# Optimization experiments

Measured on AMD Instinct MI355X. Metric: run time of the kernel, lower is better.

## Reference

```python
import jax, jax.numpy as jnp
import numpy as np

B, T, K, H, KS = 4, 2048, 128, 8, 5
DIL = 2
PAD = (KS - 1) * DIL  # left causal pad = 8


def _conv1d(x, w, dil):
    # x: [b, c_in, t], w: [c_out, c_in, ks] -> [b, c_out, t_out]
    return jax.lax.conv_general_dilated(
        x, w, window_strides=(1,), padding='VALID',
        rhs_dilation=(dil,), dimension_numbers=('NCH', 'OIH', 'NCH'))


def setup_inputs() -> dict:
    key = jax.random.key(0)
    ks = jax.random.split(key, 8)
    s = 0.05
    return {
        'x': jax.random.normal(ks[0], (B, T, K), dtype=jnp.float32),
        'Wq': jax.random.normal(ks[1], (K * H, K, KS), dtype=jnp.float32) * s,
        'bq': jax.random.normal(ks[2], (K * H,), dtype=jnp.float32) * s,
        'Wk': jax.random.normal(ks[3], (K * H, K, KS), dtype=jnp.float32) * s,
        'bk': jax.random.normal(ks[4], (K * H,), dtype=jnp.float32) * s,
        'Wv': jax.random.normal(ks[5], (K * H, K, 1), dtype=jnp.float32) * s,
        'Wu': jax.random.normal(ks[6], (K, K * H), dtype=jnp.float32) * s,
        'bu': jax.random.normal(ks[7], (K,), dtype=jnp.float32) * s,
    }


def reference(x, Wq, bq, Wk, bk, Wv, Wu, bu):
    b, t, k = x.shape
    h = Wq.shape[0] // k
    silu = jax.nn.silu

    xt = jnp.transpose(x, (0, 2, 1))               # [b, k, t]
    xp = jnp.pad(xt, ((0, 0), (0, 0), (PAD, 0)))   # causal left pad

    # dilated convs -> view(b, k, h, t) (channel split: k outer, h inner, as in torch)
    q = silu(_conv1d(xp, Wq, DIL) + bq[None, :, None]).reshape(b, k, h, t)
    kk = silu(_conv1d(xp, Wk, DIL) + bk[None, :, None]).reshape(b, k, h, t)
    v = silu(_conv1d(xt, Wv, 1)).reshape(b, k, h, t)

    # -> (b, h, t, k)
    q = jnp.transpose(q, (0, 2, 3, 1))
    kk = jnp.transpose(kk, (0, 2, 3, 1))
    v = jnp.transpose(v, (0, 2, 3, 1))

    scale = k ** 0.25
    q = q / scale
    kk = kk / scale

    # faithful to torch: transpose(1,2) -> (b,t,h,k) then contiguous view (b*h, t, k)
    q2 = jnp.transpose(q, (0, 2, 1, 3)).reshape(b * h, t, k)
    k2 = jnp.transpose(kk, (0, 2, 1, 3)).reshape(b * h, t, k)
    v2 = jnp.transpose(v, (0, 2, 1, 3)).reshape(b * h, t, k)

    weights = jnp.einsum('mtd,msd->mts', q2, k2)   # [b*h, t, t]
    causal = jnp.triu(jnp.ones((t, t), dtype=bool), 1)  # mask_next, not diag
    weights = jnp.where(causal[None], -jnp.inf, weights)
    attn = jax.nn.softmax(weights, axis=2)
    out = jnp.einsum('mts,msd->mtd', attn, v2)     # [b*h, t, k]

    out = out.reshape(b, h, t, k).transpose(0, 2, 1, 3).reshape(b, t, k * h)
    return silu(out @ Wu.T + bu)
```

## Files before the change

kernel.cpp:

```cpp
#include <hip/hip_runtime.h>
#include <hip/hip_bf16.h>
#include <stdint.h>


typedef __attribute__((ext_vector_type(8))) short bf16x8;
typedef __attribute__((ext_vector_type(4))) float f32x4;
typedef __attribute__((ext_vector_type(4))) int   i32x4;
typedef unsigned short ushort_t;

__device__ __forceinline__ unsigned short f2bf(float x){
  union{float f; unsigned u;} v; v.f = x;
  unsigned r = v.u + 0x7FFFu + ((v.u >> 16) & 1u);
  return (unsigned short)(r >> 16);
}
__device__ __forceinline__ float silu_f(float x){ return x / (1.f + __expf(-x)); }

__device__ __forceinline__ int cvt_pk_bf16(float lo, float hi){
  int r;
  asm("v_cvt_pk_bf16_f32 %0, %1, %2" : "=v"(r) : "v"(lo), "v"(hi));
  return r;
}

__device__ __forceinline__ void async_cp16(void* lds, const void* g){
  __builtin_amdgcn_global_load_lds(
      (const __attribute__((address_space(1))) unsigned int*)g,
      (__attribute__((address_space(3))) unsigned int*)lds, 16, 0, 0);
}

__global__ __launch_bounds__(256) void prep(const float* __restrict__ Wq,
                                            const float* __restrict__ Wk,
                                            const float* __restrict__ Wv,
                                            const float* __restrict__ Wu,
                                            const float* __restrict__ x,
                                            ushort_t* __restrict__ W2p,
                                            ushort_t* __restrict__ Wvp,
                                            ushort_t* __restrict__ Wub,
                                            ushort_t* __restrict__ Xpad){
  __shared__ float row[640];
  int n = blockIdx.x;
  int tid = threadIdx.x;
  if (n < 2048){
    int qk = n >> 10, h = (n >> 7) & 7, d = n & 127;
    const float* src = (qk ? Wk : Wq) + (size_t)(d*8 + h)*640;
    if (tid < 160) *(float4*)&row[tid*4] = *(const float4*)&src[tid*4];
    __syncthreads();
    for (int rp = tid; rp < 640; rp += 256){
      int j = rp >> 7, ci = rp & 127;
      W2p[(size_t)n*640 + rp] = f2bf(row[ci*5 + j]);
    }
  } else if (n < 3072){
    int co = n - 2048;
    if (tid < 32){
      float4 v = *(const float4*)&Wv[(size_t)co*128 + tid*4];
      uint2 pv;
      pv.x = (unsigned)cvt_pk_bf16(v.x, v.y);
      pv.y = (unsigned)cvt_pk_bf16(v.z, v.w);
      *(uint2*)&Wvp[(size_t)co*128 + tid*4] = pv;
    }
  } else if (n < 3200){
    int j = n - 3072;
    float4 v = *(const float4*)&Wu[(size_t)j*1024 + tid*4];
    uint2 pv;
    pv.x = (unsigned)cvt_pk_bf16(v.x, v.y);
    pv.y = (unsigned)cvt_pk_bf16(v.z, v.w);
    *(uint2*)&Wub[(size_t)j*1024 + tid*4] = pv;
  } else {
    int idx = n - 3200;
    int b = idx / 257, rblk = idx - b*257;
    int rt = rblk*8 + (tid >> 5);
    int ci4 = (tid & 31) * 4;
    int t = rt - 8;
    uint2 val; val.x = 0u; val.y = 0u;
    if (t >= 0){
      float4 v = *(const float4*)&x[((size_t)(b*2048 + t))*128 + ci4];
      val.x = (unsigned)cvt_pk_bf16(v.x, v.y);
      val.y = (unsigned)cvt_pk_bf16(v.z, v.w);
    }
    *(uint2*)&Xpad[((size_t)(b*2056 + rt))*128 + ci4] = val;
  }
}

__global__ __launch_bounds__(256) void gemm_qkv(
    const ushort_t* __restrict__ Xpad,
    const ushort_t* __restrict__ W2p,
    const ushort_t* __restrict__ Wvp,
    const float* __restrict__ bq, const float* __restrict__ bk,
    ushort_t* __restrict__ Q2, ushort_t* __restrict__ K2,
    ushort_t* __restrict__ V2t)
{
  __shared__ ushort_t As[2][128*32] __attribute__((aligned(16)));
  __shared__ ushort_t Bs[2][128*32] __attribute__((aligned(16)));
  int bt0 = blockIdx.y * 128;
  int tid = threadIdx.x;
  int w = tid >> 6, ln = tid & 63;
  int lc = ln & 15, lg = ln >> 4;
  int mi = (w & 1) * 64, nj = (w >> 1) * 64;
  int srow = ln >> 2;
  int kseg = (ln & 3) * 8;
  int b = bt0 >> 11, tl0 = bt0 & 2047;

  f32x4 acc[4][4];
  #pragma unroll
  for (int si = 0; si < 4; si++)
    #pragma unroll
    for (int sj = 0; sj < 4; sj++) acc[si][sj] = (f32x4){0.f,0.f,0.f,0.f};

  if (blockIdx.x < 16){
    int n0 = blockIdx.x * 128;
    const ushort_t* gA = Xpad + (size_t)(b*2056 + tl0 + w*32 + srow)*128 + kseg;
    const ushort_t* gB = W2p + (size_t)(n0  + w*32 + srow)*640 + kseg;

    auto stageAB = [&](int kk, int bsel){
      int j = kk >> 2, ci0 = (kk & 3) * 32;
      int r0 = kk * 32;
      const ushort_t* a0 = gA + (size_t)(2*j)*128 + ci0;
      async_cp16(&As[bsel][w*1024],       a0);
      async_cp16(&As[bsel][w*1024 + 512], a0 + 16*128);
      async_cp16(&Bs[bsel][w*1024],       gB + r0);
      async_cp16(&Bs[bsel][w*1024 + 512], gB + r0 + 16*640);
    };

    stageAB(0, 0);
    for (int kk = 0; kk < 20; kk++){
      int bsel = kk & 1;
      if (kk + 1 < 20){
        stageAB(kk + 1, bsel ^ 1);
        asm volatile("s_waitcnt vmcnt(4)\n\ts_barrier" ::: "memory");
      } else {
        asm volatile("s_waitcnt vmcnt(0)\n\ts_barrier" ::: "memory");
      }
      bf16x8 af[4], bfr[4];
      #pragma unroll
      for (int si = 0; si < 4; si++)
        af[si] = *(const bf16x8*)&As[bsel][(mi + 16*si + lc)*32 + 8*lg];
      #pragma unroll
      for (int sj = 0; sj < 4; sj++)
        bfr[sj] = *(const bf16x8*)&Bs[bsel][(nj + 16*sj + lc)*32 + 8*lg];
      #pragma unroll
      for (int si = 0; si < 4; si++)
        #pragma unroll
        for (int sj = 0; sj < 4; sj++)
          acc[si][sj] = __builtin_amdgcn_mfma_f32_16x16x32_bf16(af[si], bfr[sj],
                                                                acc[si][sj], 0,0,0);
      asm volatile("s_barrier" ::: "memory");
    }

    const float inv_scale = 0.29730177875068026f;
    int qk = n0 >> 10, h = (n0 >> 7) & 7;
    const float* bias = qk ? bk : bq;
    ushort_t* dst = qk ? K2 : Q2;
    float bv[4];
    #pragma unroll
    for (int sj = 0; sj < 4; sj++) bv[sj] = bias[(nj + 16*sj + lc)*8 + h];

    #pragma unroll
    for (int si = 0; si < 4; si++){
      int btb = bt0 + mi + 16*si + 4*lg;
      #pragma unroll
      for (int r = 0; r < 4; r++){
        int t = btb + r;
        int bb = t >> 11, tl = t & 2047;
        size_t rowoff = ((size_t)(bb*8 + (tl >> 8))*2048 + (tl & 255)*8 + h)*128;
        #pragma unroll
        for (int sj = 0; sj < 4; sj++){
          int d = nj + 16*sj + lc;
          dst[rowoff + d] = f2bf(silu_f(acc[si][sj][r] + bv[sj]) * inv_scale);
        }
      }
    }
  } else {
    int n0 = (blockIdx.x - 16) * 128;
    const ushort_t* gA = Xpad + (size_t)(b*2056 + 8 + tl0 + w*32 + srow)*128 + kseg;
    const ushort_t* gB = Wvp  + (size_t)(n0 + w*32 + srow)*128 + kseg;

    auto stageV = [&](int kk, int bsel){
      int r0 = kk * 32;
      async_cp16(&As[bsel][w*1024],       gA + r0);
      async_cp16(&As[bsel][w*1024 + 512], gA + r0 + 16*128);
      async_cp16(&Bs[bsel][w*1024],       gB + r0);
      async_cp16(&Bs[bsel][w*1024 + 512], gB + r0 + 16*128);
    };

    stageV(0, 0);
    for (int kk = 0; kk < 4; kk++){
      int bsel = kk & 1;
      if (kk + 1 < 4){
        stageV(kk + 1, bsel ^ 1);
        asm volatile("s_waitcnt vmcnt(4)\n\ts_barrier" ::: "memory");
      } else {
        asm volatile("s_waitcnt vmcnt(0)\n\ts_barrier" ::: "memory");
      }
      bf16x8 af[4], bfr[4];
      #pragma unroll
      for (int si = 0; si < 4; si++)
        af[si] = *(const bf16x8*)&As[bsel][(mi + 16*si + lc)*32 + 8*lg];
      #pragma unroll
      for (int sj = 0; sj < 4; sj++)
        bfr[sj] = *(const bf16x8*)&Bs[bsel][(nj + 16*sj + lc)*32 + 8*lg];
      #pragma unroll
      for (int si = 0; si < 4; si++)
        #pragma unroll
        for (int sj = 0; sj < 4; sj++)
          acc[si][sj] = __builtin_amdgcn_mfma_f32_16x16x32_bf16(af[si], bfr[sj],
                                                                acc[si][sj], 0,0,0);
      asm volatile("s_barrier" ::: "memory");
    }

    #pragma unroll
    for (int si = 0; si < 4; si++){
      int btb = bt0 + mi + 16*si + 4*lg;
      #pragma unroll
      for (int r = 0; r < 4; r++){
        int t = btb + r;
        int bb = t >> 11, tl = t & 2047;
        int mm = bb*8 + (tl >> 8);
        int tpb = (tl & 255)*8;
        #pragma unroll
        for (int sj = 0; sj < 4; sj++){
          int co = n0 + nj + 16*sj + lc;
          int d = co >> 3, hh = co & 7;
          V2t[((size_t)mm*128 + d)*2048 + tpb + hh] = f2bf(silu_f(acc[si][sj][r]));
        }
      }
    }
  }
}

__global__ __launch_bounds__(256) void attn(
    const ushort_t* __restrict__ Q2,
    const ushort_t* __restrict__ K2,
    const ushort_t* __restrict__ V2t,
    ushort_t* __restrict__ O2)
{
  __shared__ i32x4 kbuf[2][1024];
  __shared__ i32x4 vbuf[2][1024];

  int bid = blockIdx.x;
  int m   = ((bid & 7) << 2) | ((bid >> 3) & 3);
  int ip  = bid >> 5;
  int tid = threadIdx.x;
  int w = tid >> 6, l = tid & 63;
  int lc = l & 15, lg = l >> 4;

  int iA = 31 - ip, iB = ip;
  int ntA = iA + 1;
  const int nt = 33;

  const size_t mQ = (size_t)m * 2048;
  const ushort_t* Kbase = K2  + mQ * 128;
  const ushort_t* Vbase = V2t + (size_t)m * 128 * 2048;
  int hb = m & 7, bI = m >> 3;

  int psel[4];
  #pragma unroll
  for (int w2 = 0; w2 < 4; w2++)
    psel[w2] = ((((2*(lg & 1) + (w2 >> 1)) << 4) | lc) << 2);

  auto stage = [&](int s0, int bsel){
    const ushort_t* krow = Kbase + (size_t)(s0 + w*16 + lc)*128 + 8*lg;
    #pragma unroll
    for (int c = 0; c < 4; c++)
      async_cp16(&kbuf[bsel][(w*4 + c)*64], krow + 32*c);
    #pragma unroll
    for (int j = 0; j < 4; j++){
      int dt = w*2 + (j >> 1);
      const ushort_t* vrow = Vbase + (size_t)(dt*16 + lc)*2048
                             + s0 + (j & 1)*32 + 8*lg;
      async_cp16(&vbuf[bsel][(w*4 + j)*64], vrow);
    }
  };

  int qb = iA*64 + w*16;
  bf16x8 qfrag[4];
  {
    const ushort_t* qp = Q2 + (mQ + qb + lc)*128 + 8*lg;
    #pragma unroll
    for (int c = 0; c < 4; c++) qfrag[c] = *(const bf16x8*)(qp + 32*c);
  }
  f32x4 oacc[8];
  #pragma unroll
  for (int dt = 0; dt < 8; dt++) oacc[dt] = (f32x4){0.f,0.f,0.f,0.f};
  float lrow = 0.f;

  const float LOG2E = 1.4426950408889634f;
  const float EOFF  = -11.541560327111707f;

  stage(0, 0);

  for (int step = 0; step < nt; step++){
    if (step == ntA){
      float lt = lrow;
      lt += __shfl_xor(lt, 16);
      lt += __shfl_xor(lt, 32);
      float invl = 1.f / lt;
      size_t obase = ((size_t)(bI*2048 + qb + lc))*1024 + hb*128 + 4*lg;
      #pragma unroll
      for (int dt = 0; dt < 8; dt++){
        uint2 val;
        val.x = (unsigned)cvt_pk_bf16(oacc[dt][0]*invl, oacc[dt][1]*invl);
        val.y = (unsigned)cvt_pk_bf16(oacc[dt][2]*invl, oacc[dt][3]*invl);
        *(uint2*)&O2[obase + 16*dt] = val;
      }
      qb = iB*64 + w*16;
      const ushort_t* qp = Q2 + (mQ + qb + lc)*128 + 8*lg;
      #pragma unroll
      for (int c = 0; c < 4; c++) qfrag[c] = *(const bf16x8*)(qp + 32*c);
      #pragma unroll
      for (int dt = 0; dt < 8; dt++) oacc[dt] = (f32x4){0.f,0.f,0.f,0.f};
      lrow = 0.f;
    }
    int local = (step < ntA) ? step : step - ntA;
    bool isLast = (step == ntA - 1) || (step == nt - 1);
    int s0 = local * 64;
    int bsel = step & 1;

    if (step + 1 < nt){
      int nl = (step + 1 < ntA) ? step + 1 : step + 1 - ntA;
      stage(nl*64, bsel ^ 1);
      asm volatile("s_waitcnt vmcnt(8)\n\ts_barrier" ::: "memory");
    } else {
      asm volatile("s_waitcnt vmcnt(0)\n\ts_barrier" ::: "memory");
    }

    f32x4 sacc[4];
    #pragma unroll
    for (int st = 0; st < 4; st++){
      f32x4 a2 = (f32x4){0.f,0.f,0.f,0.f};
      #pragma unroll
      for (int c = 0; c < 4; c++){
        bf16x8 kf = *(bf16x8*)&kbuf[bsel][(st*4 + c)*64 + l];
        a2 = __builtin_amdgcn_mfma_f32_16x16x32_bf16(kf, qfrag[c], a2, 0, 0, 0);
      }
      sacc[st] = a2;
    }
    if (isLast){
      int qg = qb + lc;
      #pragma unroll
      for (int st = 0; st < 4; st++)
        #pragma unroll
        for (int r = 0; r < 4; r++){
          int sg = s0 + st*16 + 4*lg + r;
          if (sg > qg) sacc[st][r] = -1e30f;
        }
    }

    float p_[4][4];
    #pragma unroll
    for (int st = 0; st < 4; st++)
      #pragma unroll
      for (int r = 0; r < 4; r++){
        float sv = fminf(fmaf(sacc[st][r], LOG2E, EOFF), 108.f);
        float pv = __builtin_amdgcn_exp2f(sv);
        p_[st][r] = pv;
        lrow += pv;
      }

    #pragma unroll
    for (int ks = 0; ks < 2; ks++){
      int pk0[2], pk1[2];
      #pragma unroll
      for (int pa = 0; pa < 2; pa++){
        pk0[pa] = cvt_pk_bf16(p_[2*ks][2*pa],   p_[2*ks][2*pa+1]);
        pk1[pa] = cvt_pk_bf16(p_[2*ks+1][2*pa], p_[2*ks+1][2*pa+1]);
      }
      union { int i[4]; bf16x8 v; } bfr;
      #pragma unroll
      for (int w2 = 0; w2 < 4; w2++){
        int v0 = __builtin_amdgcn_ds_bpermute(psel[w2], pk0[w2 & 1]);
        int v1 = __builtin_amdgcn_ds_bpermute(psel[w2], pk1[w2 & 1]);
        bfr.i[w2] = (lg >> 1) ? v1 : v0;
      }
      #pragma unroll
      for (int dt = 0; dt < 8; dt++){
        bf16x8 vf = *(bf16x8*)&vbuf[bsel][(dt*2 + ks)*64 + l];
        oacc[dt] = __builtin_amdgcn_mfma_f32_16x16x32_bf16(vf, bfr.v, oacc[dt], 0, 0, 0);
      }
    }
    asm volatile("s_barrier" ::: "memory");
  }

  float lt = lrow;
  lt += __shfl_xor(lt, 16);
  lt += __shfl_xor(lt, 32);
  float invl = 1.f / lt;
  size_t obase = ((size_t)(bI*2048 + qb + lc))*1024 + hb*128 + 4*lg;
  #pragma unroll
  for (int dt = 0; dt < 8; dt++){
    uint2 val;
    val.x = (unsigned)cvt_pk_bf16(oacc[dt][0]*invl, oacc[dt][1]*invl);
    val.y = (unsigned)cvt_pk_bf16(oacc[dt][2]*invl, oacc[dt][3]*invl);
    *(uint2*)&O2[obase + 16*dt] = val;
  }
}

__global__ __launch_bounds__(256) void finalmm(
    const ushort_t* __restrict__ O2,
    const ushort_t* __restrict__ Wub,
    const float* __restrict__ bu,
    float* __restrict__ out)
{
  __shared__ ushort_t As[2][32*32]  __attribute__((aligned(16)));
  __shared__ ushort_t Bs[2][128*32] __attribute__((aligned(16)));
  int bt0 = blockIdx.x * 32;
  int tid = threadIdx.x;
  int w = tid >> 6, ln = tid & 63;
  int lc = ln & 15, lg = ln >> 4;
  int nj = w * 32;
  int srow = ln >> 2;
  int kseg = (ln & 3) * 8;

  f32x4 acc[2][2];
  #pragma unroll
  for (int si = 0; si < 2; si++)
    #pragma unroll
    for (int sj = 0; sj < 2; sj++) acc[si][sj] = (f32x4){0.f,0.f,0.f,0.f};

  const ushort_t* gA = O2  + (size_t)(bt0 + (w & 1)*16 + srow)*1024 + kseg;
  const ushort_t* gB = Wub + (size_t)(w*32 + srow)*1024 + kseg;

  auto stageF = [&](int kk, int bsel){
    int r0 = kk * 32;
    if (w < 2) async_cp16(&As[bsel][w*512], gA + r0);
    async_cp16(&Bs[bsel][w*1024],       gB + r0);
    async_cp16(&Bs[bsel][w*1024 + 512], gB + r0 + 16*1024);
  };

  stageF(0, 0);
  for (int kk = 0; kk < 32; kk++){
    int bsel = kk & 1;
    if (kk + 1 < 32){
      stageF(kk + 1, bsel ^ 1);
      asm volatile("s_waitcnt vmcnt(2)\n\ts_barrier" ::: "memory");
    } else {
      asm volatile("s_waitcnt vmcnt(0)\n\ts_barrier" ::: "memory");
    }
    bf16x8 af[2], bfr[2];
    #pragma unroll
    for (int si = 0; si < 2; si++)
      af[si] = *(const bf16x8*)&As[bsel][(16*si + lc)*32 + 8*lg];
    #pragma unroll
    for (int sj = 0; sj < 2; sj++)
      bfr[sj] = *(const bf16x8*)&Bs[bsel][(nj + 16*sj + lc)*32 + 8*lg];
    #pragma unroll
    for (int si = 0; si < 2; si++)
      #pragma unroll
      for (int sj = 0; sj < 2; sj++)
        acc[si][sj] = __builtin_amdgcn_mfma_f32_16x16x32_bf16(af[si], bfr[sj],
                                                              acc[si][sj], 0,0,0);
    asm volatile("s_barrier" ::: "memory");
  }

  float bv[2];
  #pragma unroll
  for (int sj = 0; sj < 2; sj++) bv[sj] = bu[nj + 16*sj + lc];
  #pragma unroll
  for (int si = 0; si < 2; si++)
    #pragma unroll
    for (int r = 0; r < 4; r++){
      int t = bt0 + 16*si + 4*lg + r;
      #pragma unroll
      for (int sj = 0; sj < 2; sj++)
        out[(size_t)t*128 + nj + 16*sj + lc] = silu_f(acc[si][sj][r] + bv[sj]);
    }
}

extern "C" void kernel_launch(void* const* d_in, const int* in_sizes, int n_in,
                              void* d_out, int out_size, void* d_ws, size_t ws_size,
                              hipStream_t stream) {
  const float* x  = (const float*)d_in[0];
  const float* Wq = (const float*)d_in[1];
  const float* bq = (const float*)d_in[2];
  const float* Wk = (const float*)d_in[3];
  const float* bk = (const float*)d_in[4];
  const float* Wv = (const float*)d_in[5];
  const float* Wu = (const float*)d_in[6];
  const float* bu = (const float*)d_in[7];
  float* out = (float*)d_out;

  char* ws = (char*)d_ws;
  ushort_t* Q2   = (ushort_t*)(ws + 0);
  ushort_t* K2   = (ushort_t*)(ws + 16777216);
  ushort_t* V2t  = (ushort_t*)(ws + 33554432);
  ushort_t* O2   = (ushort_t*)(ws + 50331648);
  ushort_t* Xpad = (ushort_t*)(ws + 67108864);
  ushort_t* W2p  = (ushort_t*)(ws + 70254592);
  ushort_t* Wvp  = (ushort_t*)(ws + 73400320);
  ushort_t* Wub  = (ushort_t*)(ws + 74448896);

  prep<<<dim3(4228, 1, 1), 256, 0, stream>>>(Wq, Wk, Wv, Wu, x,
                                             W2p, Wvp, Wub, Xpad);

  gemm_qkv<<<dim3(24, 64, 1), 256, 0, stream>>>(Xpad, W2p, Wvp, bq, bk,
                                                Q2, K2, V2t);

  attn<<<dim3(512, 1, 1), 256, 0, stream>>>(Q2, K2, V2t, O2);
  finalmm<<<dim3(256, 1, 1), 256, 0, stream>>>(O2, Wub, bu, out);
}
```

Before: 203.0 us.

## Process both paired query tiles concurrently to share K/V tile loads

The attention kernel previously walked the K/V sequence twice per block, once for the long query tile and once for the short one, staging 33 K/V tiles in total. It now loads K/V tiles only for the longer causal range and, during the first iB+1 steps, computes scores and PV products for both query tiles against the same staged tiles. This roughly halves global-to-LDS staging and barrier count per block. In exchange it doubles the accumulator and Q-fragment registers (two oacc sets of 8 f32x4), which may raise VGPR pressure and lower occupancy.

```diff
diff --git a/kernel.cpp b/kernel.cpp
--- a/kernel.cpp
+++ b/kernel.cpp
@@ -242,9 +242,10 @@
   int w = tid >> 6, l = tid & 63;
   int lc = l & 15, lg = l >> 4;
 
-  int iA = 31 - ip, iB = ip;
-  int ntA = iA + 1;
-  const int nt = 33;
+  int iA = 31 - ip;
+  int iB = ip;
+  int nsteps = iA + 1;
+  int ndual  = iB + 1;
 
   const size_t mQ = (size_t)m * 2048;
   const ushort_t* Kbase = K2  + mQ * 128;
@@ -270,126 +271,195 @@
     }
   };
 
-  int qb = iA*64 + w*16;
-  bf16x8 qfrag[4];
+  int qbA = iA*64 + w*16;
+  int qbB = iB*64 + w*16;
+  bf16x8 qf[2][4];
   {
-    const ushort_t* qp = Q2 + (mQ + qb + lc)*128 + 8*lg;
-    #pragma unroll
-    for (int c = 0; c < 4; c++) qfrag[c] = *(const bf16x8*)(qp + 32*c);
-  }
-  f32x4 oacc[8];
+    const ushort_t* qpA = Q2 + (mQ + qbA + lc)*128 + 8*lg;
+    const ushort_t* qpB = Q2 + (mQ + qbB + lc)*128 + 8*lg;
+    #pragma unroll
+    for (int c = 0; c < 4; c++){
+      qf[0][c] = *(const bf16x8*)(qpA + 32*c);
+      qf[1][c] = *(const bf16x8*)(qpB + 32*c);
+    }
+  }
+  f32x4 oacc[2][8];
   #pragma unroll
-  for (int dt = 0; dt < 8; dt++) oacc[dt] = (f32x4){0.f,0.f,0.f,0.f};
-  float lrow = 0.f;
+  for (int dt = 0; dt < 8; dt++){
+    oacc[0][dt] = (f32x4){0.f,0.f,0.f,0.f};
+    oacc[1][dt] = (f32x4){0.f,0.f,0.f,0.f};
+  }
+  float lrow0 = 0.f, lrow1 = 0.f;
 
   const float LOG2E = 1.4426950408889634f;
   const float EOFF  = -11.541560327111707f;
 
   stage(0, 0);
 
-  for (int step = 0; step < nt; step++){
-    if (step == ntA){
-      float lt = lrow;
-      lt += __shfl_xor(lt, 16);
-      lt += __shfl_xor(lt, 32);
-      float invl = 1.f / lt;
-      size_t obase = ((size_t)(bI*2048 + qb + lc))*1024 + hb*128 + 4*lg;
-      #pragma unroll
-      for (int dt = 0; dt < 8; dt++){
-        uint2 val;
-        val.x = (unsigned)cvt_pk_bf16(oacc[dt][0]*invl, oacc[dt][1]*invl);
-        val.y = (unsigned)cvt_pk_bf16(oacc[dt][2]*invl, oacc[dt][3]*invl);
-        *(uint2*)&O2[obase + 16*dt] = val;
-      }
-      qb = iB*64 + w*16;
-      const ushort_t* qp = Q2 + (mQ + qb + lc)*128 + 8*lg;
-      #pragma unroll
-      for (int c = 0; c < 4; c++) qfrag[c] = *(const bf16x8*)(qp + 32*c);
-      #pragma unroll
-      for (int dt = 0; dt < 8; dt++) oacc[dt] = (f32x4){0.f,0.f,0.f,0.f};
-      lrow = 0.f;
-    }
-    int local = (step < ntA) ? step : step - ntA;
-    bool isLast = (step == ntA - 1) || (step == nt - 1);
-    int s0 = local * 64;
-    int bsel = step & 1;
-
-    if (step + 1 < nt){
-      int nl = (step + 1 < ntA) ? step + 1 : step + 1 - ntA;
-      stage(nl*64, bsel ^ 1);
+  for (int s = 0; s < nsteps; s++){
+    int bsel = s & 1;
+    int s0 = s * 64;
+
+    if (s + 1 < nsteps){
+      stage(s0 + 64, bsel ^ 1);
       asm volatile("s_waitcnt vmcnt(8)\n\ts_barrier" ::: "memory");
     } else {
       asm volatile("s_waitcnt vmcnt(0)\n\ts_barrier" ::: "memory");
     }
 
-    f32x4 sacc[4];
-    #pragma unroll
-    for (int st = 0; st < 4; st++){
-      f32x4 a2 = (f32x4){0.f,0.f,0.f,0.f};
-      #pragma unroll
-      for (int c = 0; c < 4; c++){
-        bf16x8 kf = *(bf16x8*)&kbuf[bsel][(st*4 + c)*64 + l];
-        a2 = __builtin_amdgcn_mfma_f32_16x16x32_bf16(kf, qfrag[c], a2, 0, 0, 0);
-      }
-      sacc[st] = a2;
-    }
-    if (isLast){
-      int qg = qb + lc;
+    if (s < ndual){
+      f32x4 sacc0[4], sacc1[4];
+      #pragma unroll
+      for (int st = 0; st < 4; st++){
+        f32x4 a0 = (f32x4){0.f,0.f,0.f,0.f};
+        f32x4 a1 = (f32x4){0.f,0.f,0.f,0.f};
+        #pragma unroll
+        for (int c = 0; c < 4; c++){
+          bf16x8 kf = *(bf16x8*)&kbuf[bsel][(st*4 + c)*64 + l];
+          a0 = __builtin_amdgcn_mfma_f32_16x16x32_bf16(kf, qf[0][c], a0, 0, 0, 0);
+          a1 = __builtin_amdgcn_mfma_f32_16x16x32_bf16(kf, qf[1][c], a1, 0, 0, 0);
+        }
+        sacc0[st] = a0; sacc1[st] = a1;
+      }
+      if (s == iB){
+        int qg = qbB + lc;
+        #pragma unroll
+        for (int st = 0; st < 4; st++)
+          #pragma unroll
+          for (int r = 0; r < 4; r++){
+            int sg = s0 + st*16 + 4*lg + r;
+            if (sg > qg) sacc1[st][r] = -1e30f;
+          }
+      }
+
+      float p0_[4][4], p1_[4][4];
       #pragma unroll
       for (int st = 0; st < 4; st++)
         #pragma unroll
         for (int r = 0; r < 4; r++){
-          int sg = s0 + st*16 + 4*lg + r;
-          if (sg > qg) sacc[st][r] = -1e30f;
-        }
-    }
-
-    float p_[4][4];
-    #pragma unroll
-    for (int st = 0; st < 4; st++)
-      #pragma unroll
-      for (int r = 0; r < 4; r++){
-        float sv = fminf(fmaf(sacc[st][r], LOG2E, EOFF), 108.f);
-        float pv = __builtin_amdgcn_exp2f(sv);
-        p_[st][r] = pv;
-        lrow += pv;
-      }
-
-    #pragma unroll
-    for (int ks = 0; ks < 2; ks++){
-      int pk0[2], pk1[2];
-      #pragma unroll
-      for (int pa = 0; pa < 2; pa++){
-        pk0[pa] = cvt_pk_bf16(p_[2*ks][2*pa],   p_[2*ks][2*pa+1]);
-        pk1[pa] = cvt_pk_bf16(p_[2*ks+1][2*pa], p_[2*ks+1][2*pa+1]);
-      }
-      union { int i[4]; bf16x8 v; } bfr;
-      #pragma unroll
-      for (int w2 = 0; w2 < 4; w2++){
-        int v0 = __builtin_amdgcn_ds_bpermute(psel[w2], pk0[w2 & 1]);
-        int v1 = __builtin_amdgcn_ds_bpermute(psel[w2], pk1[w2 & 1]);
-        bfr.i[w2] = (lg >> 1) ? v1 : v0;
-      }
-      #pragma unroll
-      for (int dt = 0; dt < 8; dt++){
-        bf16x8 vf = *(bf16x8*)&vbuf[bsel][(dt*2 + ks)*64 + l];
-        oacc[dt] = __builtin_amdgcn_mfma_f32_16x16x32_bf16(vf, bfr.v, oacc[dt], 0, 0, 0);
+          float sv0 = fminf(fmaf(sacc0[st][r], LOG2E, EOFF), 108.f);
+          float pv0 = __builtin_amdgcn_exp2f(sv0);
+          p0_[st][r] = pv0;
+          lrow0 += pv0;
+          float sv1 = fminf(fmaf(sacc1[st][r], LOG2E, EOFF), 108.f);
+          float pv1 = __builtin_amdgcn_exp2f(sv1);
+          p1_[st][r] = pv1;
+          lrow1 += pv1;
+        }
+
+      #pragma unroll
+      for (int ks = 0; ks < 2; ks++){
+        int apk0[2], apk1[2], bpk0[2], bpk1[2];
+        #pragma unroll
+        for (int pa = 0; pa < 2; pa++){
+          apk0[pa] = cvt_pk_bf16(p0_[2*ks][2*pa],   p0_[2*ks][2*pa+1]);
+          apk1[pa] = cvt_pk_bf16(p0_[2*ks+1][2*pa], p0_[2*ks+1][2*pa+1]);
+          bpk0[pa] = cvt_pk_bf16(p1_[2*ks][2*pa],   p1_[2*ks][2*pa+1]);
+          bpk1[pa] = cvt_pk_bf16(p1_[2*ks+1][2*pa], p1_[2*ks+1][2*pa+1]);
+        }
+        union { int i[4]; bf16x8 v; } bfrA, bfrB;
+        #pragma unroll
+        for (int w2 = 0; w2 < 4; w2++){
+          int v0 = __builtin_amdgcn_ds_bpermute(psel[w2], apk0[w2 & 1]);
+          int v1 = __builtin_amdgcn_ds_bpermute(psel[w2], apk1[w2 & 1]);
+          bfrA.i[w2] = (lg >> 1) ? v1 : v0;
+          int u0 = __builtin_amdgcn_ds_bpermute(psel[w2], bpk0[w2 & 1]);
+          int u1 = __builtin_amdgcn_ds_bpermute(psel[w2], bpk1[w2 & 1]);
+          bfrB.i[w2] = (lg >> 1) ? u1 : u0;
+        }
+        #pragma unroll
+        for (int dt = 0; dt < 8; dt++){
+          bf16x8 vf = *(bf16x8*)&vbuf[bsel][(dt*2 + ks)*64 + l];
+          oacc[0][dt] = __builtin_amdgcn_mfma_f32_16x16x32_bf16(vf, bfrA.v, oacc[0][dt], 0, 0, 0);
+          oacc[1][dt] = __builtin_amdgcn_mfma_f32_16x16x32_bf16(vf, bfrB.v, oacc[1][dt], 0, 0, 0);
+        }
+      }
+    } else {
+      f32x4 sacc[4];
+      #pragma unroll
+      for (int st = 0; st < 4; st++){
+        f32x4 a2 = (f32x4){0.f,0.f,0.f,0.f};
+        #pragma unroll
+        for (int c = 0; c < 4; c++){
+          bf16x8 kf = *(bf16x8*)&kbuf[bsel][(st*4 + c)*64 + l];
+          a2 = __builtin_amdgcn_mfma_f32_16x16x32_bf16(kf, qf[0][c], a2, 0, 0, 0);
+        }
+        sacc[st] = a2;
+      }
+      if (s == iA){
+        int qg = qbA + lc;
+        #pragma unroll
+        for (int st = 0; st < 4; st++)
+          #pragma unroll
+          for (int r = 0; r < 4; r++){
+            int sg = s0 + st*16 + 4*lg + r;
+            if (sg > qg) sacc[st][r] = -1e30f;
+          }
+      }
+
+      float p_[4][4];
+      #pragma unroll
+      for (int st = 0; st < 4; st++)
+        #pragma unroll
+        for (int r = 0; r < 4; r++){
+          float sv = fminf(fmaf(sacc[st][r], LOG2E, EOFF), 108.f);
+          float pv = __builtin_amdgcn_exp2f(sv);
+          p_[st][r] = pv;
+          lrow0 += pv;
+        }
+
+      #pragma unroll
+      for (int ks = 0; ks < 2; ks++){
+        int pk0[2], pk1[2];
+        #pragma unroll
+        for (int pa = 0; pa < 2; pa++){
+          pk0[pa] = cvt_pk_bf16(p_[2*ks][2*pa],   p_[2*ks][2*pa+1]);
+          pk1[pa] = cvt_pk_bf16(p_[2*ks+1][2*pa], p_[2*ks+1][2*pa+1]);
+        }
+        union { int i[4]; bf16x8 v; } bfr;
+        #pragma unroll
+        for (int w2 = 0; w2 < 4; w2++){
+          int v0 = __builtin_amdgcn_ds_bpermute(psel[w2], pk0[w2 & 1]);
+          int v1 = __builtin_amdgcn_ds_bpermute(psel[w2], pk1[w2 & 1]);
+          bfr.i[w2] = (lg >> 1) ? v1 : v0;
+        }
+        #pragma unroll
+        for (int dt = 0; dt < 8; dt++){
+          bf16x8 vf = *(bf16x8*)&vbuf[bsel][(dt*2 + ks)*64 + l];
+          oacc[0][dt] = __builtin_amdgcn_mfma_f32_16x16x32_bf16(vf, bfr.v, oacc[0][dt], 0, 0, 0);
+        }
       }
     }
     asm volatile("s_barrier" ::: "memory");
   }
 
-  float lt = lrow;
-  lt += __shfl_xor(lt, 16);
-  lt += __shfl_xor(lt, 32);
-  float invl = 1.f / lt;
-  size_t obase = ((size_t)(bI*2048 + qb + lc))*1024 + hb*128 + 4*lg;
-  #pragma unroll
-  for (int dt = 0; dt < 8; dt++){
-    uint2 val;
-    val.x = (unsigned)cvt_pk_bf16(oacc[dt][0]*invl, oacc[dt][1]*invl);
-    val.y = (unsigned)cvt_pk_bf16(oacc[dt][2]*invl, oacc[dt][3]*invl);
-    *(uint2*)&O2[obase + 16*dt] = val;
+  {
+    float lt = lrow0;
+    lt += __shfl_xor(lt, 16);
+    lt += __shfl_xor(lt, 32);
+    float invl = 1.f / lt;
+    size_t obase = ((size_t)(bI*2048 + qbA + lc))*1024 + hb*128 + 4*lg;
+    #pragma unroll
+    for (int dt = 0; dt < 8; dt++){
+      uint2 val;
+      val.x = (unsigned)cvt_pk_bf16(oacc[0][dt][0]*invl, oacc[0][dt][1]*invl);
+      val.y = (unsigned)cvt_pk_bf16(oacc[0][dt][2]*invl, oacc[0][dt][3]*invl);
+      *(uint2*)&O2[obase + 16*dt] = val;
+    }
+  }
+  {
+    float lt = lrow1;
+    lt += __shfl_xor(lt, 16);
+    lt += __shfl_xor(lt, 32);
+    float invl = 1.f / lt;
+    size_t obase = ((size_t)(bI*2048 + qbB + lc))*1024 + hb*128 + 4*lg;
+    #pragma unroll
+    for (int dt = 0; dt < 8; dt++){
+      uint2 val;
+      val.x = (unsigned)cvt_pk_bf16(oacc[1][dt][0]*invl, oacc[1][dt][1]*invl);
+      val.y = (unsigned)cvt_pk_bf16(oacc[1][dt][2]*invl, oacc[1][dt][3]*invl);
+      *(uint2*)&O2[obase + 16*dt] = val;
+    }
   }
 }
 
```

Result: slower. 254.5 us (+25.3%).
